# Performance work log

Hardware: AMD Instinct MI355X
Metric: run time of the kernel (lower is better)

## Reference

```python
import jax, jax.numpy as jnp
import numpy as np

N, K, CIN, COUT = 100000, 16, 128, 128
D2 = COUT // 2
EPS = 1e-5


def setup_inputs() -> dict:
    key = jax.random.key(0)
    ks = jax.random.split(key, 12)

    def w(k, shape, fan_in):
        return (jax.random.normal(k, shape, jnp.float32) / np.sqrt(fan_in)).astype(jnp.float32)

    return {
        "xyz": jax.random.normal(ks[0], (N, 3), jnp.float32),
        "x": jax.random.normal(ks[1], (N, CIN), jnp.float32),
        "knn": jax.random.randint(ks[2], (N, K), 0, N, jnp.int32),
        "W": w(ks[3], (CIN, COUT), CIN),            # proj (no bias)
        "m1_w": w(ks[4], (3, D2), 3),                # NCA mlp1
        "m1_b": jnp.zeros((D2,), jnp.float32),
        "m2_w": w(ks[5], (D2, D2), D2),              # NCA mlp2
        "m2_b": jnp.zeros((D2,), jnp.float32),
        "m3a_w": w(ks[6], (COUT, COUT), COUT),       # NCA mlp3[0]
        "m3a_b": jnp.zeros((COUT,), jnp.float32),
        "m3b_w": w(ks[7], (COUT, COUT), COUT),       # NCA mlp3[2]
        "m3b_b": jnp.zeros((COUT,), jnp.float32),
        "gamma": jnp.ones((COUT,), jnp.float32),     # bn.weight (init=1.0)
        "beta": jnp.zeros((COUT,), jnp.float32),     # bn.bias
    }


def reference(xyz, x, knn, W, m1_w, m1_b, m2_w, m2_b, m3a_w, m3a_b, m3b_w, m3b_b, gamma, beta):
    # linear projection of features
    xp = x @ W                                   # (N, C)
    # neighbor gathers (irregular access)
    xs = xp[knn] - xp[:, None, :]                # (N, K, C)
    xyzs = xyz[knn] - xyz[:, None, :]            # (N, K, 3)
    # NCA positional MLP
    p0 = xyzs @ m1_w + m1_b                      # (N, K, C/2)
    p_local = p0.max(axis=1)                     # (N, C/2)
    p1 = p0 @ m2_w + m2_b                        # (N, K, C/2)
    pfeat = jnp.concatenate(
        [p1, jnp.broadcast_to(p_local[:, None, :], p1.shape)], axis=-1
    )                                            # (N, K, C)
    pe = jax.nn.gelu(pfeat @ m3a_w + m3a_b, approximate=False) @ m3b_w + m3b_b
    # add PE, max-aggregate over neighbors
    xs_max = (xs + pe).max(axis=1)               # (N, C)
    # BatchNorm1d (training mode: batch stats, biased variance)
    mean = xs_max.mean(axis=0)
    var = ((xs_max - mean) ** 2).mean(axis=0)
    return (xs_max - mean) / jnp.sqrt(var + EPS) * gamma + beta
```

## Files before the change

### kernel.cpp

```cpp
#include <hip/hip_runtime.h>
#include <hip/hip_bf16.h>
#include <math.h>

#define KNN 16
#define CIN 128
#define COUT 128
#define D2 64
#define EPS 1e-5f

typedef __attribute__((ext_vector_type(8))) short short8;
typedef __attribute__((ext_vector_type(4))) float f32x4;
typedef unsigned int u32;
typedef unsigned short u16;

union S8U { short8 s; u32 u[4]; };

#define MFMA16(a, b, c) __builtin_amdgcn_mfma_f32_16x16x32_bf16((a), (b), (c), 0, 0, 0)

static __device__ __forceinline__ u16 f2bf(float f) {
  __hip_bfloat16 h = __float2bfloat16(f);
  u16 u; __builtin_memcpy(&u, &h, 2); return u;
}
#if __has_builtin(__builtin_amdgcn_cvt_pk_bf16_f32)
static __device__ __forceinline__ u32 pack2(float a, float b) {
  auto r = __builtin_amdgcn_cvt_pk_bf16_f32(a, b);
  u32 u; __builtin_memcpy(&u, &r, 4); return u;
}
#else
static __device__ __forceinline__ u32 pack2(float a, float b) {
  return (u32)f2bf(a) | ((u32)f2bf(b) << 16);
}
#endif
static __device__ __forceinline__ float bf_lo(u32 u) { return __uint_as_float(u << 16); }
static __device__ __forceinline__ float bf_hi(u32 u) { return __uint_as_float(u & 0xffff0000u); }

static __device__ __forceinline__ float gelu_fast(float x) {
  float e = __builtin_amdgcn_exp2f(x * -2.4555331f);
  return x * __builtin_amdgcn_rcpf(1.0f + e);
}

template <int CTRL>
static __device__ __forceinline__ float dppmax(float v) {
  int s = __builtin_bit_cast(int, v);
  int t = __builtin_amdgcn_update_dpp(s, s, CTRL, 0xf, 0xf, true);
  return fmaxf(v, __builtin_bit_cast(float, t));
}
static __device__ __forceinline__ float rowmax16(float v) {
  v = dppmax<0xB1>(v);
  v = dppmax<0x4E>(v);
  v = dppmax<0x141>(v);
  v = dppmax<0x128>(v);
  return v;
}

__global__ __launch_bounds__(256) void k_proj(const float* __restrict__ x,
                                              const float* __restrict__ W,
                                              u32* __restrict__ xp,
                                              float* __restrict__ part, int n) {
  const int t = threadIdx.x;
  if (blockIdx.x == 0 && t < 256) part[t] = 0.f;

  __shared__ __align__(16) u32 Wf[8192];
  for (int idx = t; idx < 8192; idx += 256) {
    int f = idx >> 8, rem = idx & 255;
    int l = rem >> 2, jp = rem & 3;
    int mt = f >> 2, ks = f & 3;
    int qq = l >> 4, mm = l & 15;
    int k = ks * 32 + qq * 8 + jp * 2;
    int c = mt * 16 + mm;
    Wf[idx] = pack2(W[(size_t)k * COUT + c], W[(size_t)(k + 1) * COUT + c]);
  }
  __syncthreads();

  const int wv = t >> 6, l = t & 63;
  const int q = l >> 4, m = l & 15;
  const short8* Wf8 = (const short8*)Wf;

  for (int tile = blockIdx.x * 4 + wv; tile * 16 < n; tile += gridDim.x * 4) {
    int r0 = tile * 16;
    int rr = min(r0 + m, n - 1);
    const float4* xr = (const float4*)(x + (size_t)rr * CIN);
    S8U xf[4];
#pragma unroll
    for (int ks = 0; ks < 4; ks++) {
      float4 a = xr[ks * 8 + q * 2];
      float4 b = xr[ks * 8 + q * 2 + 1];
      xf[ks].u[0] = pack2(a.x, a.y);
      xf[ks].u[1] = pack2(a.z, a.w);
      xf[ks].u[2] = pack2(b.x, b.y);
      xf[ks].u[3] = pack2(b.z, b.w);
    }
    bool ok = (r0 + m) < n;
    size_t rowb = (size_t)(r0 + m) * 64;
#pragma unroll
    for (int mt = 0; mt < 8; mt++) {
      f32x4 acc = {0.f, 0.f, 0.f, 0.f};
      __builtin_amdgcn_s_setprio(1);
#pragma unroll
      for (int ks = 0; ks < 4; ks++)
        acc = MFMA16(Wf8[(mt * 4 + ks) * 64 + l], xf[ks].s, acc);
      __builtin_amdgcn_s_setprio(0);
      if (ok) {
        uint2 v;
        v.x = pack2(acc[0], acc[1]);
        v.y = pack2(acc[2], acc[3]);
        *(uint2*)&xp[rowb + mt * 8 + q * 2] = v;
      }
    }
  }
}

__global__ __launch_bounds__(1024, 4) void k_lfa(
    const float* __restrict__ xyz, const u32* __restrict__ xp,
    const int* __restrict__ knn,
    const float* __restrict__ m1w, const float* __restrict__ m1b,
    const float* __restrict__ m2w, const float* __restrict__ m2b,
    const float* __restrict__ m3aw, const float* __restrict__ m3ab,
    const float* __restrict__ m3bw, const float* __restrict__ m3bb,
    float* __restrict__ xsmax, float* __restrict__ part, int n) {
  __shared__ __align__(16) char lds[116992];

  const int t = threadIdx.x, wv = t >> 6, l = t & 63;
  const int q = l >> 4, m = l & 15;

  {
    u32* lds32 = (u32*)lds;
    for (int idx = t; idx < 18432; idx += 1024) {
      int f = idx >> 8, rem = idx & 255;
      int ll = rem >> 2, jp = rem & 3;
      int qq = ll >> 4, mm = ll & 15;
      int j0 = jp * 2;
      float a, b;
      if (f < 8) {
        int mt = f >> 1, s = f & 1;
        const float* p = m2w + (size_t)(s * 32 + qq * 8 + j0) * D2 + mt * 16 + mm;
        a = p[0]; b = p[D2];
      } else if (f < 40) {
        int ff = f - 8; int mt = ff >> 2, s = ff & 3;
        const float* p = m3aw + (size_t)(s * 32 + qq * 8 + j0) * COUT + mt * 16 + mm;
        a = p[0]; b = p[COUT];
      } else {
        int ff = f - 40; int mt = ff >> 2, s = ff & 3;
        const float* p = m3bw + (size_t)(s * 32 + qq * 8 + j0) * COUT + mt * 16 + mm;
        a = p[0]; b = p[COUT];
      }
      lds32[idx] = pack2(a, b);
    }
    if (t < 64) {
      int p = (t & 32) + (t & 7) * 4 + ((t >> 3) & 3);
      ((float4*)(lds + 73728))[p] = make_float4(m1w[t], m1w[64 + t], m1w[128 + t], m1b[t]);
    }
    if (t < 320) {
      float* bias = (float*)(lds + 74752);
      bias[t] = (t < 64) ? m2b[t] : (t < 192) ? m3ab[t - 64] : m3bb[t - 192];
    }
  }
  __syncthreads();

  const char* fr = lds;
  const float4* w14 = (const float4*)(lds + 73728);
  const float* bias = (const float*)(lds + 74752);
  char* sA = lds + 76032 + wv * 2560;
  char* sB = sA + 1280;

  for (int pr = blockIdx.x * 16 + wv; pr * 2 < n; pr += gridDim.x * 16) {
    const int ptA = pr * 2;
    const int ptB = ptA + 1;
    const bool hasB = ptB < n;
    const int ptBc = hasB ? ptB : ptA;
    const int kidA = knn[(size_t)ptA * KNN + m];
    const int kidB = knn[(size_t)ptBc * KNN + m];

    uint2 gA[8], gB[8];
#pragma unroll
    for (int mt = 0; mt < 8; mt++) {
      gA[mt] = *(const uint2*)(xp + (size_t)kidA * 64 + mt * 8 + q * 2);
      gB[mt] = *(const uint2*)(xp + (size_t)kidB * 64 + mt * 8 + q * 2);
    }

    float pxA = xyz[ptA * 3 + 0], pyA = xyz[ptA * 3 + 1], pzA = xyz[ptA * 3 + 2];
    float pxB = xyz[ptBc * 3 + 0], pyB = xyz[ptBc * 3 + 1], pzB = xyz[ptBc * 3 + 2];
    float axA = xyz[kidA * 3 + 0] - pxA, ayA = xyz[kidA * 3 + 1] - pyA, azA = xyz[kidA * 3 + 2] - pzA;
    float axB = xyz[kidB * 3 + 0] - pxB, ayB = xyz[kidB * 3 + 1] - pyB, azB = xyz[kidB * 3 + 2] - pzB;

    float p0A[16], p0B[16];
#pragma unroll
    for (int s = 0; s < 2; s++)
#pragma unroll
      for (int j = 0; j < 8; j++) {
        float4 w = w14[s * 32 + j * 4 + q];
        p0A[s * 8 + j] = fmaf(axA, w.x, fmaf(ayA, w.y, fmaf(azA, w.z, w.w)));
        p0B[s * 8 + j] = fmaf(axB, w.x, fmaf(ayB, w.y, fmaf(azB, w.z, w.w)));
      }
    S8U bp0A[2], bp0B[2], bplA[2], bplB[2];
#pragma unroll
    for (int s = 0; s < 2; s++)
#pragma unroll
      for (int jj = 0; jj < 4; jj++) {
        bp0A[s].u[jj] = pack2(p0A[s * 8 + 2 * jj], p0A[s * 8 + 2 * jj + 1]);
        bp0B[s].u[jj] = pack2(p0B[s * 8 + 2 * jj], p0B[s * 8 + 2 * jj + 1]);
      }
#pragma unroll
    for (int i = 0; i < 16; i++) { p0A[i] = rowmax16(p0A[i]); p0B[i] = rowmax16(p0B[i]); }
#pragma unroll
    for (int s = 0; s < 2; s++)
#pragma unroll
      for (int jj = 0; jj < 4; jj++) {
        bplA[s].u[jj] = pack2(p0A[s * 8 + 2 * jj], p0A[s * 8 + 2 * jj + 1]);
        bplB[s].u[jj] = pack2(p0B[s * 8 + 2 * jj], p0B[s * 8 + 2 * jj + 1]);
      }

    short8 bpfA[2], bpfB[2];
#pragma unroll
    for (int s = 0; s < 2; s++) {
#pragma unroll
      for (int h = 0; h < 2; h++) {
        int mt = 2 * s + h;
        float4 bb = *(const float4*)&bias[mt * 16 + q * 4];
        f32x4 accA = {bb.x, bb.y, bb.z, bb.w};
        f32x4 accB = accA;
        __builtin_amdgcn_s_setprio(1);
#pragma unroll
        for (int ks = 0; ks < 2; ks++) {
          short8 af = *(const short8*)(fr + (mt * 2 + ks) * 1024 + l * 16);
          accA = MFMA16(af, bp0A[ks].s, accA);
          accB = MFMA16(af, bp0B[ks].s, accB);
        }
        __builtin_amdgcn_s_setprio(0);
        uint2 wA; wA.x = pack2(accA[0], accA[1]); wA.y = pack2(accA[2], accA[3]);
        uint2 wB; wB.x = pack2(accB[0], accB[1]); wB.y = pack2(accB[2], accB[3]);
        *(uint2*)(sA + m * 80 + h * 32 + q * 8) = wA;
        *(uint2*)(sB + m * 80 + h * 32 + q * 8) = wB;
      }
      bpfA[s] = *(const short8*)(sA + m * 80 + q * 16);
      bpfB[s] = *(const short8*)(sB + m * 80 + q * 16);
    }

    short8 bgA[4], bgB[4];
#pragma unroll
    for (int s = 0; s < 4; s++) {
#pragma unroll
      for (int h = 0; h < 2; h++) {
        int mt = 2 * s + h;
        float4 bb = *(const float4*)&bias[64 + mt * 16 + q * 4];
        f32x4 accA = {bb.x, bb.y, bb.z, bb.w};
        f32x4 accB = accA;
        __builtin_amdgcn_s_setprio(1);
#pragma unroll
        for (int ks = 0; ks < 4; ks++) {
          short8 af = *(const short8*)(fr + (8 + mt * 4 + ks) * 1024 + l * 16);
          short8 bA = (ks == 0) ? bpfA[0] : (ks == 1) ? bpfA[1] : (ks == 2) ? bplA[0].s : bplA[1].s;
          short8 bB = (ks == 0) ? bpfB[0] : (ks == 1) ? bpfB[1] : (ks == 2) ? bplB[0].s : bplB[1].s;
          accA = MFMA16(af, bA, accA);
          accB = MFMA16(af, bB, accB);
        }
        __builtin_amdgcn_s_setprio(0);
        uint2 wA; wA.x = pack2(gelu_fast(accA[0]), gelu_fast(accA[1]));
        wA.y = pack2(gelu_fast(accA[2]), gelu_fast(accA[3]));
        uint2 wB; wB.x = pack2(gelu_fast(accB[0]), gelu_fast(accB[1]));
        wB.y = pack2(gelu_fast(accB[2]), gelu_fast(accB[3]));
        *(uint2*)(sA + m * 80 + h * 32 + q * 8) = wA;
        *(uint2*)(sB + m * 80 + h * 32 + q * 8) = wB;
      }
      bgA[s] = *(const short8*)(sA + m * 80 + q * 16);
      bgB[s] = *(const short8*)(sB + m * 80 + q * 16);
    }

#pragma unroll
    for (int mt = 0; mt < 8; mt++) {
      float4 bb = *(const float4*)&bias[192 + mt * 16 + q * 4];
      f32x4 accA = {bb.x, bb.y, bb.z, bb.w};
      f32x4 accB = accA;
      __builtin_amdgcn_s_setprio(1);
#pragma unroll
      for (int ks = 0; ks < 4; ks++) {
        short8 af = *(const short8*)(fr + (40 + mt * 4 + ks) * 1024 + l * 16);
        accA = MFMA16(af, bgA[ks], accA);
        accB = MFMA16(af, bgB[ks], accB);
      }
      __builtin_amdgcn_s_setprio(0);
      {
        uint2 sf = *(const uint2*)(xp + (size_t)ptA * 64 + mt * 8 + q * 2);
        float v0 = bf_lo(gA[mt].x) + accA[0];
        float v1 = bf_hi(gA[mt].x) + accA[1];
        float v2 = bf_lo(gA[mt].y) + accA[2];
        float v3 = bf_hi(gA[mt].y) + accA[3];
        v0 = rowmax16(v0); v1 = rowmax16(v1); v2 = rowmax16(v2); v3 = rowmax16(v3);
        if (m == 0) {
          float4 o = make_float4(v0 - bf_lo(sf.x), v1 - bf_hi(sf.x),
                                 v2 - bf_lo(sf.y), v3 - bf_hi(sf.y));
          *(float4*)&xsmax[(size_t)ptA * COUT + mt * 16 + q * 4] = o;
        }
      }
      {
        uint2 sf = *(const uint2*)(xp + (size_t)ptBc * 64 + mt * 8 + q * 2);
        float v0 = bf_lo(gB[mt].x) + accB[0];
        float v1 = bf_hi(gB[mt].x) + accB[1];
        float v2 = bf_lo(gB[mt].y) + accB[2];
        float v3 = bf_hi(gB[mt].y) + accB[3];
        v0 = rowmax16(v0); v1 = rowmax16(v1); v2 = rowmax16(v2); v3 = rowmax16(v3);
        if (hasB && m == 0) {
          float4 o = make_float4(v0 - bf_lo(sf.x), v1 - bf_hi(sf.x),
                                 v2 - bf_lo(sf.y), v3 - bf_hi(sf.y));
          *(float4*)&xsmax[(size_t)ptB * COUT + mt * 16 + q * 4] = o;
        }
      }
    }
  }

  __syncthreads();
  {
    float s0 = 0.f, s1 = 0.f, q0 = 0.f, q1 = 0.f;
    for (int pr = blockIdx.x * 16 + wv; pr * 2 < n; pr += gridDim.x * 16) {
      int ptA = pr * 2, ptB = ptA + 1;
      float2 a = *(const float2*)&xsmax[(size_t)ptA * COUT + l * 2];
      s0 += a.x; s1 += a.y; q0 = fmaf(a.x, a.x, q0); q1 = fmaf(a.y, a.y, q1);
      if (ptB < n) {
        float2 b = *(const float2*)&xsmax[(size_t)ptB * COUT + l * 2];
        s0 += b.x; s1 += b.y; q0 = fmaf(b.x, b.x, q0); q1 = fmaf(b.y, b.y, q1);
      }
    }
    float* slice = (float*)(lds + 76032) + wv * 256;
    slice[l * 2 + 0] = s0;
    slice[l * 2 + 1] = s1;
    slice[128 + l * 2 + 0] = q0;
    slice[128 + l * 2 + 1] = q1;
  }
  __syncthreads();
  if (t < 256) {
    const float* slices = (const float*)(lds + 76032);
    float s = 0.f;
#pragma unroll
    for (int w = 0; w < 16; w++) s += slices[w * 256 + t];
    atomicAdd(&part[t], s);
  }
}

__global__ __launch_bounds__(256) void k_bnnorm(const float* __restrict__ xs,
                                                const float* __restrict__ part,
                                                const float* __restrict__ gamma,
                                                const float* __restrict__ beta,
                                                float* __restrict__ out, int n) {
  __shared__ float ms[256];
  int t = threadIdx.x;
  if (t < 128) {
    float inv_n = 1.0f / (float)n;
    float mean = part[t] * inv_n;
    float var = part[128 + t] * inv_n - mean * mean;
    ms[t] = mean;
    ms[128 + t] = rsqrtf(var + EPS);
  }
  __syncthreads();
  size_t i = (size_t)blockIdx.x * 256 + t;
  size_t total4 = (size_t)n * (COUT / 4);
  if (i >= total4) return;
  int c = (int)((i * 4) & (COUT - 1));
  float4 v = ((const float4*)xs)[i];
  float4 mn = *(const float4*)&ms[c];
  float4 iv = *(const float4*)&ms[128 + c];
  float4 gm = *(const float4*)&gamma[c];
  float4 bt = *(const float4*)&beta[c];
  float4 o;
  o.x = (v.x - mn.x) * iv.x * gm.x + bt.x;
  o.y = (v.y - mn.y) * iv.y * gm.y + bt.y;
  o.z = (v.z - mn.z) * iv.z * gm.z + bt.z;
  o.w = (v.w - mn.w) * iv.w * gm.w + bt.w;
  ((float4*)out)[i] = o;
}

extern "C" void kernel_launch(void* const* d_in, const int* in_sizes, int n_in,
                              void* d_out, int out_size, void* d_ws, size_t ws_size,
                              hipStream_t stream) {
  const float* xyz = (const float*)d_in[0];
  const float* x = (const float*)d_in[1];
  const int* knn = (const int*)d_in[2];
  const float* W = (const float*)d_in[3];
  const float* m1w = (const float*)d_in[4];
  const float* m1b = (const float*)d_in[5];
  const float* m2w = (const float*)d_in[6];
  const float* m2b = (const float*)d_in[7];
  const float* m3aw = (const float*)d_in[8];
  const float* m3ab = (const float*)d_in[9];
  const float* m3bw = (const float*)d_in[10];
  const float* m3bb = (const float*)d_in[11];
  const float* gamma = (const float*)d_in[12];
  const float* beta = (const float*)d_in[13];
  float* out = (float*)d_out;

  int n = in_sizes[0] / 3;

  char* ws = (char*)d_ws;
  u32* xp = (u32*)ws;
  size_t o1 = (((size_t)n * 256 + 255) & ~(size_t)255);
  float* xsm = (float*)(ws + o1);
  size_t o2 = o1 + (((size_t)n * 512 + 255) & ~(size_t)255);
  float* part = (float*)(ws + o2);

  k_proj<<<1024, 256, 0, stream>>>(x, W, xp, part, n);
  k_lfa<<<256, 1024, 0, stream>>>(xyz, xp, knn, m1w, m1b, m2w, m2b,
                                  m3aw, m3ab, m3bw, m3bb, xsm, part, n);
  k_bnnorm<<<(int)(((size_t)n * (COUT / 4) + 255) / 256), 256, 0, stream>>>(
      xsm, part, gamma, beta, out, n);
}
```

Measured before the change: 468.2 us.

## Fuse BatchNorm stats and normalization into LFA kernel via cooperative grid sync

Turns the LFA kernel into a cooperative launch with grid-wide syncs, so the BatchNorm statistics reduction and the normalization pass run inside the same kernel. The separate k_bnnorm launch goes away. The stats pass is reorganized so each block reads a contiguous row range with float4 loads, and the normalize pass reuses that same range. This removes one kernel launch and the gap between kernels, at the cost of two grid barriers and some extra cooperative-launch overhead.

```diff
diff --git a/kernel.cpp b/kernel.cpp
--- a/kernel.cpp
+++ b/kernel.cpp
@@ -1,6 +1,9 @@
 #include <hip/hip_runtime.h>
 #include <hip/hip_bf16.h>
+#include <hip/hip_cooperative_groups.h>
 #include <math.h>
+
+namespace cg = cooperative_groups;
 
 #define KNN 16
 #define CIN 128
@@ -117,7 +120,9 @@
     const float* __restrict__ m2w, const float* __restrict__ m2b,
     const float* __restrict__ m3aw, const float* __restrict__ m3ab,
     const float* __restrict__ m3bw, const float* __restrict__ m3bb,
-    float* __restrict__ xsmax, float* __restrict__ part, int n) {
+    float* __restrict__ xsmax, float* __restrict__ part,
+    const float* __restrict__ gamma, const float* __restrict__ beta,
+    float* __restrict__ out, int n) {
   __shared__ __align__(16) char lds[116992];
 
   const int t = threadIdx.x, wv = t >> 6, l = t & 63;
@@ -308,64 +313,68 @@
     }
   }
 
+  cg::this_grid().sync();
+
+  const int npb = (n + gridDim.x - 1) / gridDim.x;
+  const int r0 = blockIdx.x * npb;
+  const int r1 = min(n, r0 + npb);
+  const int row_off = t >> 5;
+  const int c4 = t & 31;
+  {
+    float4 s = make_float4(0.f, 0.f, 0.f, 0.f);
+    float4 qd = make_float4(0.f, 0.f, 0.f, 0.f);
+    for (int r = r0 + row_off; r < r1; r += 32) {
+      float4 v = *(const float4*)&xsmax[(size_t)r * COUT + c4 * 4];
+      s.x += v.x; s.y += v.y; s.z += v.z; s.w += v.w;
+      qd.x = fmaf(v.x, v.x, qd.x); qd.y = fmaf(v.y, v.y, qd.y);
+      qd.z = fmaf(v.z, v.z, qd.z); qd.w = fmaf(v.w, v.w, qd.w);
+    }
+    float* red = (float*)lds;
+    *(float4*)&red[t * 4] = s;
+    *(float4*)&red[4096 + t * 4] = qd;
+  }
   __syncthreads();
-  {
-    float s0 = 0.f, s1 = 0.f, q0 = 0.f, q1 = 0.f;
-    for (int pr = blockIdx.x * 16 + wv; pr * 2 < n; pr += gridDim.x * 16) {
-      int ptA = pr * 2, ptB = ptA + 1;
-      float2 a = *(const float2*)&xsmax[(size_t)ptA * COUT + l * 2];
-      s0 += a.x; s1 += a.y; q0 = fmaf(a.x, a.x, q0); q1 = fmaf(a.y, a.y, q1);
-      if (ptB < n) {
-        float2 b = *(const float2*)&xsmax[(size_t)ptB * COUT + l * 2];
-        s0 += b.x; s1 += b.y; q0 = fmaf(b.x, b.x, q0); q1 = fmaf(b.y, b.y, q1);
-      }
-    }
-    float* slice = (float*)(lds + 76032) + wv * 256;
-    slice[l * 2 + 0] = s0;
-    slice[l * 2 + 1] = s1;
-    slice[128 + l * 2 + 0] = q0;
-    slice[128 + l * 2 + 1] = q1;
-  }
-  __syncthreads();
-  if (t < 256) {
-    const float* slices = (const float*)(lds + 76032);
-    float s = 0.f;
-#pragma unroll
-    for (int w = 0; w < 16; w++) s += slices[w * 256 + t];
-    atomicAdd(&part[t], s);
-  }
-}
-
-__global__ __launch_bounds__(256) void k_bnnorm(const float* __restrict__ xs,
-                                                const float* __restrict__ part,
-                                                const float* __restrict__ gamma,
-                                                const float* __restrict__ beta,
-                                                float* __restrict__ out, int n) {
-  __shared__ float ms[256];
-  int t = threadIdx.x;
+  if (t < 128) {
+    const float* red = (const float*)lds;
+    float ss = 0.f, qq = 0.f;
+    int base = (t >> 2) * 4 + (t & 3);
+#pragma unroll
+    for (int ro = 0; ro < 32; ro++) {
+      ss += red[ro * 128 + base];
+      qq += red[4096 + ro * 128 + base];
+    }
+    atomicAdd(&part[t], ss);
+    atomicAdd(&part[128 + t], qq);
+  }
+  __threadfence();
+
+  cg::this_grid().sync();
+
+  float* msp = (float*)(lds + 32768);
   if (t < 128) {
     float inv_n = 1.0f / (float)n;
     float mean = part[t] * inv_n;
     float var = part[128 + t] * inv_n - mean * mean;
-    ms[t] = mean;
-    ms[128 + t] = rsqrtf(var + EPS);
+    msp[t] = mean;
+    msp[128 + t] = rsqrtf(var + EPS);
   }
   __syncthreads();
-  size_t i = (size_t)blockIdx.x * 256 + t;
-  size_t total4 = (size_t)n * (COUT / 4);
-  if (i >= total4) return;
-  int c = (int)((i * 4) & (COUT - 1));
-  float4 v = ((const float4*)xs)[i];
-  float4 mn = *(const float4*)&ms[c];
-  float4 iv = *(const float4*)&ms[128 + c];
-  float4 gm = *(const float4*)&gamma[c];
-  float4 bt = *(const float4*)&beta[c];
-  float4 o;
-  o.x = (v.x - mn.x) * iv.x * gm.x + bt.x;
-  o.y = (v.y - mn.y) * iv.y * gm.y + bt.y;
-  o.z = (v.z - mn.z) * iv.z * gm.z + bt.z;
-  o.w = (v.w - mn.w) * iv.w * gm.w + bt.w;
-  ((float4*)out)[i] = o;
+  {
+    int c = c4 * 4;
+    float4 mn = *(const float4*)&msp[c];
+    float4 iv = *(const float4*)&msp[128 + c];
+    float4 gm = *(const float4*)&gamma[c];
+    float4 bt = *(const float4*)&beta[c];
+    for (int r = r0 + row_off; r < r1; r += 32) {
+      float4 v = *(const float4*)&xsmax[(size_t)r * COUT + c];
+      float4 o;
+      o.x = (v.x - mn.x) * iv.x * gm.x + bt.x;
+      o.y = (v.y - mn.y) * iv.y * gm.y + bt.y;
+      o.z = (v.z - mn.z) * iv.z * gm.z + bt.z;
+      o.w = (v.w - mn.w) * iv.w * gm.w + bt.w;
+      *(float4*)&out[(size_t)r * COUT + c] = o;
+    }
+  }
 }
 
 extern "C" void kernel_launch(void* const* d_in, const int* in_sizes, int n_in,
@@ -397,8 +406,11 @@
   float* part = (float*)(ws + o2);
 
   k_proj<<<1024, 256, 0, stream>>>(x, W, xp, part, n);
-  k_lfa<<<256, 1024, 0, stream>>>(xyz, xp, knn, m1w, m1b, m2w, m2b,
-                                  m3aw, m3ab, m3bw, m3bb, xsm, part, n);
-  k_bnnorm<<<(int)(((size_t)n * (COUT / 4) + 255) / 256), 256, 0, stream>>>(
-      xsm, part, gamma, beta, out, n);
-}
+
+  void* args[] = {(void*)&xyz, (void*)&xp, (void*)&knn,
+                  (void*)&m1w, (void*)&m1b, (void*)&m2w, (void*)&m2b,
+                  (void*)&m3aw, (void*)&m3ab, (void*)&m3bw, (void*)&m3bb,
+                  (void*)&xsm, (void*)&part, (void*)&gamma, (void*)&beta,
+                  (void*)&out, (void*)&n};
+  hipLaunchCooperativeKernel((void*)k_lfa, dim3(256), dim3(1024), args, 0, stream);
+}
```

Result: slower. 593.8 us (+26.8%).
